# Kernel tuning notes

Hardware: AMD Instinct MI355X
Metric: run time of the kernel (lower is better)

The kernel has to match this reference:

```python
import jax, jax.numpy as jnp
import numpy as np

N = 50000
E = 800000
NFEAT = 128
NHID = 128
NCLASS = 8
BN_EPS = 1e-5
NORM_EPS = 1e-12


def _xavier(key, out_f, in_f):
    lim = float(np.sqrt(6.0 / (in_f + out_f)))
    return jax.random.uniform(key, (out_f, in_f), jnp.float32, -lim, lim)


def setup_inputs() -> dict:
    key = jax.random.key(0)
    ks = jax.random.split(key, 10)
    x = jax.random.normal(ks[0], (N, NFEAT), jnp.float32)
    edge_index = jax.random.randint(ks[1], (2, E), 0, N, jnp.int64)
    return {
        "x": x,
        "edge_index": edge_index,
        # conv1: lin_l (neighbor branch, has bias), lin_r (root branch, no bias)
        "W1l": _xavier(ks[2], NHID, NFEAT),
        "b1l": jnp.zeros((NHID,), jnp.float32),
        "W1r": _xavier(ks[3], NHID, NFEAT),
        # BatchNorm1d(nhid)
        "bn_gamma": jnp.ones((NHID,), jnp.float32),
        "bn_beta": jnp.zeros((NHID,), jnp.float32),
        # conv2
        "W2l": _xavier(ks[4], NHID, NHID),
        "b2l": jnp.zeros((NHID,), jnp.float32),
        "W2r": _xavier(ks[5], NHID, NHID),
        # fc
        "Wfc": _xavier(ks[6], NCLASS, NHID),
        "bfc": jnp.zeros((NCLASS,), jnp.float32),
    }


def _sage_conv(x, src, dst, inv_deg, Wl, bl, Wr):
    # gather neighbor features along edges, scatter-mean into destination nodes
    msg = x[src]                                            # [E, F]
    agg = jax.ops.segment_sum(msg, dst, num_segments=N)      # [N, F]
    agg = agg * inv_deg[:, None]                             # mean aggregation
    out = agg @ Wl.T + bl + x @ Wr.T                         # lin_l(agg) + lin_r(x)
    # L2 normalize per node (normalize=True)
    norm = jnp.sqrt(jnp.sum(out * out, axis=-1, keepdims=True))
    return out / jnp.maximum(norm, NORM_EPS)


def reference(x, edge_index, W1l, b1l, W1r, bn_gamma, bn_beta, W2l, b2l, W2r, Wfc, bfc):
    src, dst = edge_index[0], edge_index[1]
    deg = jax.ops.segment_sum(jnp.ones((E,), x.dtype), dst, num_segments=N)
    inv_deg = jnp.where(deg > 0, 1.0 / jnp.maximum(deg, 1.0), 0.0)

    h = _sage_conv(x, src, dst, inv_deg, W1l, b1l, W1r)

    # transition: ReLU -> BatchNorm1d (batch stats, biased var) -> Dropout (identity, eval)
    h = jax.nn.relu(h)
    mu = jnp.mean(h, axis=0)
    var = jnp.mean((h - mu) ** 2, axis=0)
    h = (h - mu) * jax.lax.rsqrt(var + BN_EPS) * bn_gamma + bn_beta

    h = _sage_conv(h, src, dst, inv_deg, W2l, b2l, W2r)
    return h @ Wfc.T + bfc
```

## Files before the change

kernel.cpp:

```cpp
#include <hip/hip_runtime.h>
#include <hip/hip_bf16.h>

#define NF 128
#define CAP 64

typedef float f4 __attribute__((ext_vector_type(4)));
typedef short s16x8 __attribute__((ext_vector_type(8)));
typedef unsigned short u16x8 __attribute__((ext_vector_type(8)));

static __device__ __forceinline__ unsigned short f2b(float f) {
    union { float f; unsigned u; } c; c.f = f;
    unsigned r = c.u + 0x7fffu + ((c.u >> 16) & 1u);
    return (unsigned short)(r >> 16);
}
static __device__ __forceinline__ float blo(unsigned v) { return __uint_as_float(v << 16); }
static __device__ __forceinline__ float bhi(unsigned v) { return __uint_as_float(v & 0xffff0000u); }

__global__ __launch_bounds__(256) void k_prep(int* __restrict__ zp, int nwords, int ZB,
                                              int SB,
                                              unsigned* __restrict__ csr32, int csrWords,
                                              const float* __restrict__ x,
                                              unsigned* __restrict__ out32, int N,
                                              const float* __restrict__ w0,
                                              const float* __restrict__ w1,
                                              const float* __restrict__ w2,
                                              unsigned short* __restrict__ wt) {
    int b = blockIdx.x;
    int S = N + 1;
    int CV2 = (S * 64 + 255) / 256;
    if (b < ZB) {
        int i = b * 256 + threadIdx.x;
        if (i < nwords) zp[i] = 0;
    } else if (b < ZB + SB) {
        int i = (b - ZB) * 256 + threadIdx.x;
        unsigned sv = ((unsigned)N << 16) | (unsigned)N;
        if (i < csrWords) csr32[i] = sv;
    } else if (b < ZB + SB + CV2) {
        int i = (b - ZB - SB) * 256 + threadIdx.x;
        if (i >= S * 64) return;
        int n = i >> 6, l = i & 63;
        int s = l >> 4, li = l & 15;
        unsigned pv = 0;
        if (n < N) {
            float2 v = *(const float2*)(x + (size_t)n * NF + l * 2);
            pv = (unsigned)f2b(v.x) | ((unsigned)f2b(v.y) << 16);
        }
        out32[(size_t)s * S * 16 + (size_t)n * 16 + li] = pv;
    } else {
        int t = (b - ZB - SB - CV2) * 256 + threadIdx.x;
        if (t >= 6144) return;
        int mat = t >> 11, rem = t & 2047;
        int col = rem >> 4, ks = (rem >> 2) & 3, qq = rem & 3;
        const float* W = (mat == 0) ? w0 : (mat == 1) ? w1 : w2;
        int layer = (mat == 2) ? 1 : 0, half = (mat == 1) ? 1 : 0;
        const float* src = W + col * NF + ks * 32 + qq * 8;
        u16x8 d;
#pragma unroll
        for (int j = 0; j < 8; ++j) d[j] = f2b(src[j]);
        *(u16x8*)(wt + layer * 65536 + (half * 4 + ks) * 4096 + (col >> 4) * 512 +
                  (qq * 16 + (col & 15)) * 8) = d;
    }
}

__global__ __launch_bounds__(256) void k_fill(const int* __restrict__ ei, int E,
                                              int* __restrict__ cnt,
                                              unsigned short* __restrict__ csr,
                                              int nper) {
    int b = blockIdx.x;
    int i = (b >> 3) * 256 + threadIdx.x;
    if (i >= E) return;
    int d = ei[E + i];
    int lo = (b & 7) * nper;
    if (d >= lo && d < lo + nper) {
        int p = atomicAdd(&cnt[d], 1);
        csr[(size_t)d * CAP + p] = (unsigned short)ei[i];
    }
}

__global__ __launch_bounds__(256) void k_prep_w2(const float* __restrict__ bnSum,
                                                 const float* __restrict__ bnSq,
                                                 const float* __restrict__ gamma,
                                                 const float* __restrict__ beta,
                                                 const float* __restrict__ w2r,
                                                 const float* __restrict__ b2l,
                                                 unsigned short* __restrict__ wtL2,
                                                 float* __restrict__ bias2,
                                                 float* __restrict__ sbn,
                                                 float* __restrict__ bbn, float n) {
    __shared__ float sl[128], bl[128];
    int tid = threadIdx.x;
    if (tid < 128) {
        float su = 0.f, sq = 0.f;
#pragma unroll
        for (int s = 0; s < 8; ++s) { su += bnSum[s * 128 + tid]; sq += bnSq[s * 128 + tid]; }
        float mu = su / n;
        float var = fmaxf(sq / n - mu * mu, 0.f);
        float s = gamma[tid] / sqrtf(var + 1e-5f);
        sl[tid] = s;
        bl[tid] = beta[tid] - mu * s;
    }
    __syncthreads();
    if (blockIdx.x < 8) {
        int t = blockIdx.x * 256 + tid;
        int col = t >> 4, ks = (t >> 2) & 3, qq = t & 3;
        int k0 = ks * 32 + qq * 8;
        u16x8 d;
#pragma unroll
        for (int j = 0; j < 8; ++j) d[j] = f2b(w2r[col * NF + k0 + j] * sl[k0 + j]);
        *(u16x8*)(wtL2 + (4 + ks) * 4096 + (col >> 4) * 512 +
                  (qq * 16 + (col & 15)) * 8) = d;
    } else {
        if (tid < NF) {
            float s = b2l[tid];
            for (int k = 0; k < NF; ++k) s += w2r[tid * NF + k] * bl[k];
            bias2[tid] = s;
            sbn[tid] = sl[tid];
            bbn[tid] = bl[tid];
        }
    }
}

template <bool TR>
__global__ __launch_bounds__(256) void k_agg(const uint4* __restrict__ T4all,
                                             const unsigned short* __restrict__ csr,
                                             const int* __restrict__ deg,
                                             const float* __restrict__ sbn,
                                             const float* __restrict__ bbn,
                                             uint4* __restrict__ outT4, int N) {
    int b = blockIdx.x;
    int S = N + 1;
    int s = (b & 7) >> 1;
    int chunk = (b >> 3) * 2 + (b & 1);
    int tid = threadIdx.x;
    int wid = tid >> 6, lane = tid & 63, g = lane >> 4, li = lane & 15;
    int node = chunk * 16 + wid * 4 + g;
    if (node >= N) return;
    int cnt = deg[node];
    int cntR = (cnt + 15) & ~15;
    int nb = li >> 2, fq = li & 3;
    const uint4* T4 = T4all + (size_t)s * S * 4;
    const unsigned short* cp = csr + (size_t)node * CAP;
    float a0 = 0, a1 = 0, a2 = 0, a3 = 0, a4 = 0, a5 = 0, a6 = 0, a7 = 0;
    for (int j = 0; j < cntR; j += 16) {
        int sA = cp[j + nb], sB = cp[j + 4 + nb], sC = cp[j + 8 + nb], sD = cp[j + 12 + nb];
        uint4 vA = T4[(size_t)sA * 4 + fq];
        uint4 vB = T4[(size_t)sB * 4 + fq];
        uint4 vC = T4[(size_t)sC * 4 + fq];
        uint4 vD = T4[(size_t)sD * 4 + fq];
        a0 += (blo(vA.x) + blo(vB.x)) + (blo(vC.x) + blo(vD.x));
        a1 += (bhi(vA.x) + bhi(vB.x)) + (bhi(vC.x) + bhi(vD.x));
        a2 += (blo(vA.y) + blo(vB.y)) + (blo(vC.y) + blo(vD.y));
        a3 += (bhi(vA.y) + bhi(vB.y)) + (bhi(vC.y) + bhi(vD.y));
        a4 += (blo(vA.z) + blo(vB.z)) + (blo(vC.z) + blo(vD.z));
        a5 += (bhi(vA.z) + bhi(vB.z)) + (bhi(vC.z) + bhi(vD.z));
        a6 += (blo(vA.w) + blo(vB.w)) + (blo(vC.w) + blo(vD.w));
        a7 += (bhi(vA.w) + bhi(vB.w)) + (bhi(vC.w) + bhi(vD.w));
    }
    a0 += __shfl_xor(a0, 4); a1 += __shfl_xor(a1, 4);
    a2 += __shfl_xor(a2, 4); a3 += __shfl_xor(a3, 4);
    a4 += __shfl_xor(a4, 4); a5 += __shfl_xor(a5, 4);
    a6 += __shfl_xor(a6, 4); a7 += __shfl_xor(a7, 4);
    a0 += __shfl_xor(a0, 8); a1 += __shfl_xor(a1, 8);
    a2 += __shfl_xor(a2, 8); a3 += __shfl_xor(a3, 8);
    a4 += __shfl_xor(a4, 8); a5 += __shfl_xor(a5, 8);
    a6 += __shfl_xor(a6, 8); a7 += __shfl_xor(a7, 8);
    if (li < 4) {
        float id = (cnt > 0) ? 1.0f / (float)cnt : 0.f;
        float r[8] = {a0 * id, a1 * id, a2 * id, a3 * id,
                      a4 * id, a5 * id, a6 * id, a7 * id};
        if (TR) {
            if (cnt > 0) {
                const float2* sc2 = (const float2*)(sbn + s * 32 + fq * 8);
                const float2* bc2 = (const float2*)(bbn + s * 32 + fq * 8);
#pragma unroll
                for (int i = 0; i < 4; ++i) {
                    float2 sc = sc2[i], bc = bc2[i];
                    r[2 * i]     = r[2 * i]     * sc.x + bc.x;
                    r[2 * i + 1] = r[2 * i + 1] * sc.y + bc.y;
                }
            }
        }
        uint4 p;
        p.x = (unsigned)f2b(r[0]) | ((unsigned)f2b(r[1]) << 16);
        p.y = (unsigned)f2b(r[2]) | ((unsigned)f2b(r[3]) << 16);
        p.z = (unsigned)f2b(r[4]) | ((unsigned)f2b(r[5]) << 16);
        p.w = (unsigned)f2b(r[6]) | ((unsigned)f2b(r[7]) << 16);
        outT4[((size_t)s * S + node) * 4 + fq] = p;
    }
}

template <int MODE>
__global__ __launch_bounds__(256, 2) void k_lin(
    const unsigned short* __restrict__ aggB,
    const unsigned short* __restrict__ src2,
    const unsigned short* __restrict__ wt,
    const float* __restrict__ bias,
    const float* __restrict__ wfc, const float* __restrict__ bfc,
    unsigned short* __restrict__ outb,
    float* __restrict__ outf,
    float* __restrict__ bnSum, float* __restrict__ bnSq, int N) {
    __shared__ __align__(16) unsigned short wlds[32768];
    __shared__ float sbuf[1024];

    int tid = threadIdx.x;
    int S = N + 1;
    int lane = tid & 63;
    int q = lane >> 4, m = lane & 15;
    int wv = tid >> 6;

    s16x8 afr[2][8];
#pragma unroll
    for (int t = 0; t < 2; ++t) {
        int rb = blockIdx.x * 128 + t * 64 + wv * 16;
        int r = rb + m; if (r >= N) r = N - 1;
        size_t rr = (size_t)r * 32 + q * 8;
#pragma unroll
        for (int ks = 0; ks < 4; ++ks)
            afr[t][ks] = *(const s16x8*)(aggB + (size_t)ks * S * 32 + rr);
#pragma unroll
        for (int ks = 0; ks < 4; ++ks)
            afr[t][4 + ks] = *(const s16x8*)(src2 + (size_t)ks * S * 32 + rr);
    }
    {
        const f4* wsrc4 = (const f4*)wt;
        f4* wd4 = (f4*)wlds;
#pragma unroll
        for (int it = 0; it < 16; ++it) wd4[tid + it * 256] = wsrc4[tid + it * 256];
    }
    if constexpr (MODE == 1) {
        if (tid < 256) sbuf[tid] = 0.f;
    } else {
        *(f4*)&sbuf[tid * 4] = ((const f4*)wfc)[tid];
    }
    __syncthreads();

    const unsigned short* wb = wlds + lane * 8;

#pragma unroll
    for (int t = 0; t < 2; ++t) {
        int row_base = blockIdx.x * 128 + t * 64 + wv * 16;
        f4 acc[8];
#pragma unroll
        for (int c = 0; c < 8; ++c) acc[c] = (f4){0.f, 0.f, 0.f, 0.f};
#pragma unroll
        for (int ks = 0; ks < 8; ++ks) {
#pragma unroll
            for (int c = 0; c < 8; ++c) {
                s16x8 bfr = *(const s16x8*)(wb + ks * 4096 + c * 512);
                acc[c] = __builtin_amdgcn_mfma_f32_16x16x32_bf16(afr[t][ks], bfr, acc[c], 0, 0, 0);
            }
        }
#pragma unroll
        for (int c = 0; c < 8; ++c) {
            float b = bias[c * 16 + m];
#pragma unroll
            for (int i = 0; i < 4; ++i) acc[c][i] += b;
        }
        float ss[4];
#pragma unroll
        for (int i = 0; i < 4; ++i) {
            float s = 0.f;
#pragma unroll
            for (int c = 0; c < 8; ++c) s += acc[c][i] * acc[c][i];
            s += __shfl_xor(s, 1); s += __shfl_xor(s, 2);
            s += __shfl_xor(s, 4); s += __shfl_xor(s, 8);
            ss[i] = 1.0f / fmaxf(sqrtf(s), 1e-12f);
        }
#pragma unroll
        for (int c = 0; c < 8; ++c)
#pragma unroll
            for (int i = 0; i < 4; ++i) acc[c][i] *= ss[i];

        if constexpr (MODE == 1) {
#pragma unroll
            for (int c = 0; c < 8; ++c)
#pragma unroll
                for (int i = 0; i < 4; ++i) acc[c][i] = fmaxf(acc[c][i], 0.f);
#pragma unroll
            for (int i = 0; i < 4; ++i) {
                int row = row_base + q * 4 + i;
                if (row <= N) {
#pragma unroll
                    for (int c = 0; c < 8; ++c)
                        outb[(size_t)(c >> 1) * S * 32 + (size_t)row * 32 + (c & 1) * 16 + m] =
                            (row < N) ? f2b(acc[c][i]) : (unsigned short)0;
                }
            }
            float su[8], sq[8];
#pragma unroll
            for (int c = 0; c < 8; ++c) { su[c] = 0.f; sq[c] = 0.f; }
#pragma unroll
            for (int i = 0; i < 4; ++i) {
                bool vi = (row_base + q * 4 + i) < N;
#pragma unroll
                for (int c = 0; c < 8; ++c) {
                    float u = vi ? acc[c][i] : 0.f;
                    su[c] += u; sq[c] += u * u;
                }
            }
#pragma unroll
            for (int c = 0; c < 8; ++c) {
                su[c] += __shfl_xor(su[c], 16); su[c] += __shfl_xor(su[c], 32);
                sq[c] += __shfl_xor(sq[c], 16); sq[c] += __shfl_xor(sq[c], 32);
            }
            if (lane < 16) {
#pragma unroll
                for (int c = 0; c < 8; ++c) {
                    atomicAdd(&sbuf[c * 16 + m], su[c]);
                    atomicAdd(&sbuf[128 + c * 16 + m], sq[c]);
                }
            }
        } else {
            float o[8][4];
#pragma unroll
            for (int cls = 0; cls < 8; ++cls)
#pragma unroll
                for (int i = 0; i < 4; ++i) o[cls][i] = 0.f;
#pragma unroll
            for (int cls = 0; cls < 8; ++cls) {
#pragma unroll
                for (int c = 0; c < 8; ++c) {
                    float wv2 = sbuf[cls * NF + c * 16 + m];
#pragma unroll
                    for (int i = 0; i < 4; ++i) o[cls][i] += acc[c][i] * wv2;
                }
#pragma unroll
                for (int i = 0; i < 4; ++i) {
                    float tt = o[cls][i];
                    tt += __shfl_xor(tt, 1); tt += __shfl_xor(tt, 2);
                    tt += __shfl_xor(tt, 4); tt += __shfl_xor(tt, 8);
                    o[cls][i] = tt;
                }
            }
            float sel[4] = {0.f, 0.f, 0.f, 0.f};
#pragma unroll
            for (int cls = 0; cls < 8; ++cls) {
                bool p = (m == cls);
#pragma unroll
                for (int i = 0; i < 4; ++i) sel[i] = p ? o[cls][i] : sel[i];
            }
            if (m < 8) {
                float bb = bfc[m];
#pragma unroll
                for (int i = 0; i < 4; ++i) {
                    int row = row_base + q * 4 + i;
                    if (row < N) outf[(size_t)row * 8 + m] = sel[i] + bb;
                }
            }
        }
    }

    if constexpr (MODE == 1) {
        __syncthreads();
        int shard = (blockIdx.x & 7) * 128;
        if (tid < 128)      atomicAdd(&bnSum[shard + tid], sbuf[tid]);
        else if (tid < 256) atomicAdd(&bnSq[shard + tid - 128], sbuf[tid]);
    }
}

extern "C" void kernel_launch(void* const* d_in, const int* in_sizes, int n_in,
                              void* d_out, int out_size, void* d_ws, size_t ws_size,
                              hipStream_t stream) {
    const float* x   = (const float*)d_in[0];
    const int*   ei  = (const int*)d_in[1];
    const float* W1l = (const float*)d_in[2];
    const float* b1l = (const float*)d_in[3];
    const float* W1r = (const float*)d_in[4];
    const float* gam = (const float*)d_in[5];
    const float* bet = (const float*)d_in[6];
    const float* W2l = (const float*)d_in[7];
    const float* b2l = (const float*)d_in[8];
    const float* W2r = (const float*)d_in[9];
    const float* Wfc = (const float*)d_in[10];
    const float* bfc = (const float*)d_in[11];
    int N = in_sizes[0] / NF;
    int E = in_sizes[1] / 2;
    int S = N + 1;

    char* w = (char*)d_ws;
    size_t o = 0;
#define ALO(nbytes) (o = (o + 255) & ~(size_t)255, o += (nbytes), (w + o - (nbytes)))
    int* cnt    = (int*)ALO((size_t)N * 4);
    float* bnSum = (float*)ALO(4096);
    float* bnSq  = (float*)ALO(4096);
    size_t zwords = o / 4;
    unsigned short* csr = (unsigned short*)ALO((size_t)N * CAP * 2);
    unsigned short* wt  = (unsigned short*)ALO((size_t)2 * 65536 * 2);
    float* sbn   = (float*)ALO(512);
    float* bbn   = (float*)ALO(512);
    float* bias2 = (float*)ALO(512);
    unsigned short* xb   = (unsigned short*)ALO((size_t)S * NF * 2);
    unsigned short* aggB = (unsigned short*)ALO((size_t)S * NF * 2);
    unsigned short* h1b  = (unsigned short*)ALO((size_t)S * NF * 2);
#undef ALO
    (void)ws_size; (void)n_in; (void)out_size;

    int EB8 = ((E + 255) / 256) * 8;
    int nper = (N + 7) / 8;
    int aggBlocks = ((N + 31) / 32) * 8;
    int LB2 = (N + 127) / 128;
    int CV2 = (S * 64 + 255) / 256;
    int ZB = (int)((zwords + 255) / 256);
    int csrWords = N * CAP / 2;
    int SB = (csrWords + 255) / 256;

    k_prep<<<ZB + SB + CV2 + 24, 256, 0, stream>>>((int*)d_ws, (int)zwords, ZB, SB,
                                                   (unsigned*)csr, csrWords,
                                                   x, (unsigned*)xb, N, W1l, W1r, W2l, wt);
    k_fill<<<EB8, 256, 0, stream>>>(ei, E, cnt, csr, nper);

    k_agg<false><<<aggBlocks, 256, 0, stream>>>((const uint4*)xb, csr, cnt,
                                                nullptr, nullptr, (uint4*)aggB, N);
    k_lin<1><<<LB2, 256, 0, stream>>>(aggB, xb, wt, b1l, nullptr, nullptr,
                                      h1b, nullptr, bnSum, bnSq, N);
    k_prep_w2<<<9, 256, 0, stream>>>(bnSum, bnSq, gam, bet, W2r, b2l,
                                     wt + 65536, bias2, sbn, bbn, (float)N);
    k_agg<true><<<aggBlocks, 256, 0, stream>>>((const uint4*)h1b, csr, cnt,
                                               sbn, bbn, (uint4*)aggB, N);
    k_lin<2><<<LB2, 256, 0, stream>>>(aggB, h1b, wt + 65536, bias2, Wfc, bfc,
                                      nullptr, (float*)d_out, nullptr, nullptr, N);
}
```

Measured before the change: 152.5 us.

## Halve k_lin tile and stage weights in two LDS halves for occupancy

k_lin now handles 64 rows per block instead of 128, with one A-fragment set per wave instead of two. It loads the 128x256 bf16 weight matrix into a 32KB LDS buffer in two halves, each followed by a barrier. This cuts LDS and register use so four blocks can fit per CU, and doubles the grid size. The cost is that every block reloads the full weight matrix, so weight traffic per row doubles, and each block adds two extra barriers.

Result: no change. 150.9 us (-1.1%).

```diff
diff --git a/kernel.cpp b/kernel.cpp
--- a/kernel.cpp
+++ b/kernel.cpp
@@ -190,7 +190,7 @@
 }
 
 template <int MODE>
-__global__ __launch_bounds__(256, 2) void k_lin(
+__global__ __launch_bounds__(256, 4) void k_lin(
     const unsigned short* __restrict__ aggB,
     const unsigned short* __restrict__ src2,
     const unsigned short* __restrict__ wt,
@@ -199,7 +199,7 @@
     unsigned short* __restrict__ outb,
     float* __restrict__ outf,
     float* __restrict__ bnSum, float* __restrict__ bnSq, int N) {
-    __shared__ __align__(16) unsigned short wlds[32768];
+    __shared__ __align__(16) unsigned short wlds[16384];
     __shared__ float sbuf[1024];
 
     int tid = threadIdx.x;
@@ -207,154 +207,149 @@
     int lane = tid & 63;
     int q = lane >> 4, m = lane & 15;
     int wv = tid >> 6;
-
-    s16x8 afr[2][8];
-#pragma unroll
-    for (int t = 0; t < 2; ++t) {
-        int rb = blockIdx.x * 128 + t * 64 + wv * 16;
-        int r = rb + m; if (r >= N) r = N - 1;
-        size_t rr = (size_t)r * 32 + q * 8;
-#pragma unroll
-        for (int ks = 0; ks < 4; ++ks)
-            afr[t][ks] = *(const s16x8*)(aggB + (size_t)ks * S * 32 + rr);
-#pragma unroll
-        for (int ks = 0; ks < 4; ++ks)
-            afr[t][4 + ks] = *(const s16x8*)(src2 + (size_t)ks * S * 32 + rr);
-    }
-    {
-        const f4* wsrc4 = (const f4*)wt;
-        f4* wd4 = (f4*)wlds;
-#pragma unroll
-        for (int it = 0; it < 16; ++it) wd4[tid + it * 256] = wsrc4[tid + it * 256];
-    }
+    int row_base = blockIdx.x * 64 + wv * 16;
+
+    int r = row_base + m; if (r >= N) r = N - 1;
+    size_t rr = (size_t)r * 32 + q * 8;
+    s16x8 afr[8];
+#pragma unroll
+    for (int ks = 0; ks < 4; ++ks)
+        afr[ks] = *(const s16x8*)(aggB + (size_t)ks * S * 32 + rr);
+#pragma unroll
+    for (int ks = 0; ks < 4; ++ks)
+        afr[4 + ks] = *(const s16x8*)(src2 + (size_t)ks * S * 32 + rr);
+
     if constexpr (MODE == 1) {
         if (tid < 256) sbuf[tid] = 0.f;
     } else {
         *(f4*)&sbuf[tid * 4] = ((const f4*)wfc)[tid];
     }
-    __syncthreads();
+
+    f4 acc[8];
+#pragma unroll
+    for (int c = 0; c < 8; ++c) acc[c] = (f4){0.f, 0.f, 0.f, 0.f};
 
     const unsigned short* wb = wlds + lane * 8;
-
-#pragma unroll
-    for (int t = 0; t < 2; ++t) {
-        int row_base = blockIdx.x * 128 + t * 64 + wv * 16;
-        f4 acc[8];
-#pragma unroll
-        for (int c = 0; c < 8; ++c) acc[c] = (f4){0.f, 0.f, 0.f, 0.f};
-#pragma unroll
-        for (int ks = 0; ks < 8; ++ks) {
+#pragma unroll
+    for (int h = 0; h < 2; ++h) {
+        const f4* wsrc4 = (const f4*)(wt + h * 16384);
+        f4* wd4 = (f4*)wlds;
+#pragma unroll
+        for (int it = 0; it < 8; ++it) wd4[tid + it * 256] = wsrc4[tid + it * 256];
+        __syncthreads();
+#pragma unroll
+        for (int ks = 0; ks < 4; ++ks) {
 #pragma unroll
             for (int c = 0; c < 8; ++c) {
                 s16x8 bfr = *(const s16x8*)(wb + ks * 4096 + c * 512);
-                acc[c] = __builtin_amdgcn_mfma_f32_16x16x32_bf16(afr[t][ks], bfr, acc[c], 0, 0, 0);
+                acc[c] = __builtin_amdgcn_mfma_f32_16x16x32_bf16(afr[h * 4 + ks], bfr,
+                                                                 acc[c], 0, 0, 0);
+            }
+        }
+        __syncthreads();
+    }
+
+#pragma unroll
+    for (int c = 0; c < 8; ++c) {
+        float b = bias[c * 16 + m];
+#pragma unroll
+        for (int i = 0; i < 4; ++i) acc[c][i] += b;
+    }
+    float ss[4];
+#pragma unroll
+    for (int i = 0; i < 4; ++i) {
+        float s = 0.f;
+#pragma unroll
+        for (int c = 0; c < 8; ++c) s += acc[c][i] * acc[c][i];
+        s += __shfl_xor(s, 1); s += __shfl_xor(s, 2);
+        s += __shfl_xor(s, 4); s += __shfl_xor(s, 8);
+        ss[i] = 1.0f / fmaxf(sqrtf(s), 1e-12f);
+    }
+#pragma unroll
+    for (int c = 0; c < 8; ++c)
+#pragma unroll
+        for (int i = 0; i < 4; ++i) acc[c][i] *= ss[i];
+
+    if constexpr (MODE == 1) {
+#pragma unroll
+        for (int c = 0; c < 8; ++c)
+#pragma unroll
+            for (int i = 0; i < 4; ++i) acc[c][i] = fmaxf(acc[c][i], 0.f);
+#pragma unroll
+        for (int i = 0; i < 4; ++i) {
+            int row = row_base + q * 4 + i;
+            if (row <= N) {
+#pragma unroll
+                for (int c = 0; c < 8; ++c)
+                    outb[(size_t)(c >> 1) * S * 32 + (size_t)row * 32 + (c & 1) * 16 + m] =
+                        (row < N) ? f2b(acc[c][i]) : (unsigned short)0;
+            }
+        }
+        float su[8], sq[8];
+#pragma unroll
+        for (int c = 0; c < 8; ++c) { su[c] = 0.f; sq[c] = 0.f; }
+#pragma unroll
+        for (int i = 0; i < 4; ++i) {
+            bool vi = (row_base + q * 4 + i) < N;
+#pragma unroll
+            for (int c = 0; c < 8; ++c) {
+                float u = vi ? acc[c][i] : 0.f;
+                su[c] += u; sq[c] += u * u;
             }
         }
 #pragma unroll
         for (int c = 0; c < 8; ++c) {
-            float b = bias[c * 16 + m];
-#pragma unroll
-            for (int i = 0; i < 4; ++i) acc[c][i] += b;
-        }
-        float ss[4];
-#pragma unroll
-        for (int i = 0; i < 4; ++i) {
-            float s = 0.f;
-#pragma unroll
-            for (int c = 0; c < 8; ++c) s += acc[c][i] * acc[c][i];
-            s += __shfl_xor(s, 1); s += __shfl_xor(s, 2);
-            s += __shfl_xor(s, 4); s += __shfl_xor(s, 8);
-            ss[i] = 1.0f / fmaxf(sqrtf(s), 1e-12f);
-        }
-#pragma unroll
-        for (int c = 0; c < 8; ++c)
-#pragma unroll
-            for (int i = 0; i < 4; ++i) acc[c][i] *= ss[i];
-
-        if constexpr (MODE == 1) {
-#pragma unroll
-            for (int c = 0; c < 8; ++c)
-#pragma unroll
-                for (int i = 0; i < 4; ++i) acc[c][i] = fmaxf(acc[c][i], 0.f);
-#pragma unroll
-            for (int i = 0; i < 4; ++i) {
-                int row = row_base + q * 4 + i;
-                if (row <= N) {
-#pragma unroll
-                    for (int c = 0; c < 8; ++c)
-                        outb[(size_t)(c >> 1) * S * 32 + (size_t)row * 32 + (c & 1) * 16 + m] =
-                            (row < N) ? f2b(acc[c][i]) : (unsigned short)0;
-                }
-            }
-            float su[8], sq[8];
-#pragma unroll
-            for (int c = 0; c < 8; ++c) { su[c] = 0.f; sq[c] = 0.f; }
-#pragma unroll
-            for (int i = 0; i < 4; ++i) {
-                bool vi = (row_base + q * 4 + i) < N;
-#pragma unroll
-                for (int c = 0; c < 8; ++c) {
-                    float u = vi ? acc[c][i] : 0.f;
-                    su[c] += u; sq[c] += u * u;
-                }
-            }
+            su[c] += __shfl_xor(su[c], 16); su[c] += __shfl_xor(su[c], 32);
+            sq[c] += __shfl_xor(sq[c], 16); sq[c] += __shfl_xor(sq[c], 32);
+        }
+        if (lane < 16) {
 #pragma unroll
             for (int c = 0; c < 8; ++c) {
-                su[c] += __shfl_xor(su[c], 16); su[c] += __shfl_xor(su[c], 32);
-                sq[c] += __shfl_xor(sq[c], 16); sq[c] += __shfl_xor(sq[c], 32);
-            }
-            if (lane < 16) {
-#pragma unroll
-                for (int c = 0; c < 8; ++c) {
-                    atomicAdd(&sbuf[c * 16 + m], su[c]);
-                    atomicAdd(&sbuf[128 + c * 16 + m], sq[c]);
-                }
-            }
-        } else {
-            float o[8][4];
-#pragma unroll
-            for (int cls = 0; cls < 8; ++cls)
-#pragma unroll
-                for (int i = 0; i < 4; ++i) o[cls][i] = 0.f;
-#pragma unroll
-            for (int cls = 0; cls < 8; ++cls) {
-#pragma unroll
-                for (int c = 0; c < 8; ++c) {
-                    float wv2 = sbuf[cls * NF + c * 16 + m];
-#pragma unroll
-                    for (int i = 0; i < 4; ++i) o[cls][i] += acc[c][i] * wv2;
-                }
-#pragma unroll
-                for (int i = 0; i < 4; ++i) {
-                    float tt = o[cls][i];
-                    tt += __shfl_xor(tt, 1); tt += __shfl_xor(tt, 2);
-                    tt += __shfl_xor(tt, 4); tt += __shfl_xor(tt, 8);
-                    o[cls][i] = tt;
-                }
-            }
-            float sel[4] = {0.f, 0.f, 0.f, 0.f};
-#pragma unroll
-            for (int cls = 0; cls < 8; ++cls) {
-                bool p = (m == cls);
-#pragma unroll
-                for (int i = 0; i < 4; ++i) sel[i] = p ? o[cls][i] : sel[i];
-            }
-            if (m < 8) {
-                float bb = bfc[m];
-#pragma unroll
-                for (int i = 0; i < 4; ++i) {
-                    int row = row_base + q * 4 + i;
-                    if (row < N) outf[(size_t)row * 8 + m] = sel[i] + bb;
-                }
-            }
-        }
-    }
-
-    if constexpr (MODE == 1) {
+                atomicAdd(&sbuf[c * 16 + m], su[c]);
+                atomicAdd(&sbuf[128 + c * 16 + m], sq[c]);
+            }
+        }
         __syncthreads();
         int shard = (blockIdx.x & 7) * 128;
         if (tid < 128)      atomicAdd(&bnSum[shard + tid], sbuf[tid]);
         else if (tid < 256) atomicAdd(&bnSq[shard + tid - 128], sbuf[tid]);
+    } else {
+        float o[8][4];
+#pragma unroll
+        for (int cls = 0; cls < 8; ++cls)
+#pragma unroll
+            for (int i = 0; i < 4; ++i) o[cls][i] = 0.f;
+#pragma unroll
+        for (int cls = 0; cls < 8; ++cls) {
+#pragma unroll
+            for (int c = 0; c < 8; ++c) {
+                float wv2 = sbuf[cls * NF + c * 16 + m];
+#pragma unroll
+                for (int i = 0; i < 4; ++i) o[cls][i] += acc[c][i] * wv2;
+            }
+#pragma unroll
+            for (int i = 0; i < 4; ++i) {
+                float tt = o[cls][i];
+                tt += __shfl_xor(tt, 1); tt += __shfl_xor(tt, 2);
+                tt += __shfl_xor(tt, 4); tt += __shfl_xor(tt, 8);
+                o[cls][i] = tt;
+            }
+        }
+        float sel[4] = {0.f, 0.f, 0.f, 0.f};
+#pragma unroll
+        for (int cls = 0; cls < 8; ++cls) {
+            bool p = (m == cls);
+#pragma unroll
+            for (int i = 0; i < 4; ++i) sel[i] = p ? o[cls][i] : sel[i];
+        }
+        if (m < 8) {
+            float bb = bfc[m];
+#pragma unroll
+            for (int i = 0; i < 4; ++i) {
+                int row = row_base + q * 4 + i;
+                if (row < N) outf[(size_t)row * 8 + m] = sel[i] + bb;
+            }
+        }
     }
 }
 
@@ -398,7 +393,7 @@
     int EB8 = ((E + 255) / 256) * 8;
     int nper = (N + 7) / 8;
     int aggBlocks = ((N + 31) / 32) * 8;
-    int LB2 = (N + 127) / 128;
+    int LB = (N + 63) / 64;
     int CV2 = (S * 64 + 255) / 256;
     int ZB = (int)((zwords + 255) / 256);
     int csrWords = N * CAP / 2;
@@ -411,12 +406,12 @@
 
     k_agg<false><<<aggBlocks, 256, 0, stream>>>((const uint4*)xb, csr, cnt,
                                                 nullptr, nullptr, (uint4*)aggB, N);
-    k_lin<1><<<LB2, 256, 0, stream>>>(aggB, xb, wt, b1l, nullptr, nullptr,
-                                      h1b, nullptr, bnSum, bnSq, N);
+    k_lin<1><<<LB, 256, 0, stream>>>(aggB, xb, wt, b1l, nullptr, nullptr,
+                                     h1b, nullptr, bnSum, bnSq, N);
     k_prep_w2<<<9, 256, 0, stream>>>(bnSum, bnSq, gam, bet, W2r, b2l,
                                      wt + 65536, bias2, sbn, bbn, (float)N);
     k_agg<true><<<aggBlocks, 256, 0, stream>>>((const uint4*)h1b, csr, cnt,
                                                sbn, bbn, (uint4*)aggB, N);
-    k_lin<2><<<LB2, 256, 0, stream>>>(aggB, h1b, wt + 65536, bias2, Wfc, bfc,
-                                      nullptr, (float*)d_out, nullptr, nullptr, N);
-}
+    k_lin<2><<<LB, 256, 0, stream>>>(aggB, h1b, wt + 65536, bias2, Wfc, bfc,
+                                     nullptr, (float*)d_out, nullptr, nullptr, N);
+}
```
